# Kernel optimization log

Measured on AMD Instinct MI355X. Metric: run time of the kernel, lower is better.

## Reference

```python
import jax, jax.numpy as jnp
import numpy as np

B = 16; DIM = 256; HEADS = 8; GRID = 64; WS = 8; NQ = 8; POOL = 4
HD = DIM // HEADS
SCALE = HD ** -0.5


def _rel_pos_index(ws):
    coords = np.stack(np.meshgrid(np.arange(ws), np.arange(ws), indexing='ij'))  # (2, ws, ws)
    cf = coords.reshape(2, -1)
    rel = (cf[:, :, None] - cf[:, None, :]).transpose(1, 2, 0).copy()
    rel[:, :, 0] += ws - 1
    rel[:, :, 1] += ws - 1
    rel[:, :, 0] *= 2 * ws - 1
    return rel.sum(-1)  # (ws*ws, ws*ws) int


def layernorm(x, g, b, eps=1e-5):
    m = x.mean(-1, keepdims=True)
    v = ((x - m) ** 2).mean(-1, keepdims=True)
    return (x - m) / jnp.sqrt(v + eps) * g + b


def linear(x, w, b):
    # torch Linear: y = x @ W.T + b, W is (out, in)
    return jnp.einsum('...i,oi->...o', x, w) + b


def setup_inputs() -> dict:
    key = jax.random.key(0)
    ks = iter(jax.random.split(key, 40))
    r = lambda shp, s=0.02: jax.random.normal(next(ks), shp, jnp.float32) * s
    C = DIM
    return {
        'x': jax.random.normal(next(ks), (B, GRID * GRID, C), jnp.float32),
        'query_tokens': r((1, NQ, C)),
        'kproj_w': r((C, C)), 'kproj_b': r((C,)),
        'kbn_g': jnp.ones((C,)), 'kbn_b': jnp.zeros((C,)),
        'kbn_m': jnp.zeros((C,)), 'kbn_v': jnp.ones((C,)),
        'vproj_w': r((C, C)), 'vproj_b': r((C,)),
        'vbn_g': jnp.ones((C,)), 'vbn_b': jnp.zeros((C,)),
        'vbn_m': jnp.zeros((C,)), 'vbn_v': jnp.ones((C,)),
        'ck_w': r((C, C)), 'ck_b': r((C,)),
        'cv_w': r((C, C)), 'cv_b': r((C,)),
        'rpb_table': r(((2 * WS - 1) ** 2, HEADS)),
        'qkv_w': r((3 * C, C)), 'qkv_b': r((3 * C,)),
        'proj_w': r((C, C)), 'proj_b': r((C,)),
        'n1_g': jnp.ones((C,)), 'n1_b': jnp.zeros((C,)),
        'n2_g': jnp.ones((C,)), 'n2_b': jnp.zeros((C,)),
        'fc1_w': r((4 * C, C)), 'fc1_b': r((4 * C,)),
        'fc2_w': r((C, 4 * C)), 'fc2_b': r((C,)),
    }


def reference(x, query_tokens, kproj_w, kproj_b, kbn_g, kbn_b, kbn_m, kbn_v,
              vproj_w, vproj_b, vbn_g, vbn_b, vbn_m, vbn_v,
              ck_w, ck_b, cv_w, cv_b, rpb_table, qkv_w, qkv_b, proj_w, proj_b,
              n1_g, n1_b, n2_g, n2_b, fc1_w, fc1_b, fc2_w, fc2_b):
    Bx, N, C = x.shape
    shortcut = x
    xn = layernorm(x, n1_g, n1_b)

    # ---- global cross-attention pooling path ----
    x2d = xn.reshape(Bx, GRID, GRID, C).transpose(0, 3, 1, 2)  # B,C,H,W
    hp = GRID // POOL
    pooled = x2d.reshape(Bx, C, hp, POOL, hp, POOL).mean((3, 5))  # B,C,hp,hp

    def proj_bn(p, w, b, g, bt, m, v):
        y = jnp.einsum('oc,bchw->bohw', w, p) + b[None, :, None, None]
        y = (y - m[None, :, None, None]) / jnp.sqrt(v + 1e-5)[None, :, None, None]
        y = y * g[None, :, None, None] + bt[None, :, None, None]
        return y.reshape(Bx, C, hp * hp).transpose(0, 2, 1)  # B, hp*hp, C

    k = proj_bn(pooled, kproj_w, kproj_b, kbn_g, kbn_b, kbn_m, kbn_v)
    v = proj_bn(pooled, vproj_w, vproj_b, vbn_g, vbn_b, vbn_m, vbn_v)
    q = jnp.broadcast_to(query_tokens, (Bx, NQ, C))
    qh = q.reshape(Bx, NQ, HEADS, HD).transpose(0, 2, 1, 3)
    kh = k.reshape(Bx, -1, HEADS, HD).transpose(0, 2, 1, 3)
    vh = v.reshape(Bx, -1, HEADS, HD).transpose(0, 2, 1, 3)
    a = jax.nn.softmax(jnp.einsum('bhqd,bhkd->bhqk', qh, kh) * SCALE, axis=-1)
    qout = jnp.einsum('bhqk,bhkd->bhqd', a, vh).transpose(0, 2, 1, 3).reshape(Bx, NQ, C)
    gk = linear(qout + q, ck_w, ck_b)  # B, NQ, C
    gv = linear(qout + q, cv_w, cv_b)

    # ---- window partition ----
    nw = GRID // WS
    xw = xn.reshape(Bx, nw, WS, nw, WS, C).transpose(0, 1, 3, 2, 4, 5).reshape(Bx * nw * nw, WS * WS, C)
    B_, Nw = Bx * nw * nw, WS * WS
    qkv = linear(xw, qkv_w, qkv_b).reshape(B_, Nw, 3, HEADS, HD).transpose(2, 0, 3, 1, 4)
    wq, wk, wv = qkv[0], qkv[1], qkv[2]  # B_, H, Nw, HD

    gkh = jnp.broadcast_to(gk[:, None], (Bx, nw * nw, NQ, C)).reshape(B_, NQ, HEADS, HD).transpose(0, 2, 1, 3)
    gvh = jnp.broadcast_to(gv[:, None], (Bx, nw * nw, NQ, C)).reshape(B_, NQ, HEADS, HD).transpose(0, 2, 1, 3)
    wk = jnp.concatenate([wk, gkh], axis=2)  # kv_len = Nw + NQ
    wv = jnp.concatenate([wv, gvh], axis=2)

    attn = jnp.einsum('bhqd,bhkd->bhqk', wq * SCALE, wk)  # B_, H, Nw, Nw+NQ
    rpi = _rel_pos_index(WS)
    bias = rpb_table[rpi.reshape(-1)].reshape(Nw, Nw, HEADS).transpose(2, 0, 1)  # H, Nw, Nw
    attn = attn.at[:, :, :, :Nw].add(bias[None])
    attn = jax.nn.softmax(attn, axis=-1)
    out = jnp.einsum('bhqk,bhkd->bhqd', attn, wv).transpose(0, 2, 1, 3).reshape(B_, Nw, C)
    out = linear(out, proj_w, proj_b)

    # window reverse
    out = out.reshape(Bx, nw, nw, WS, WS, C).transpose(0, 1, 3, 2, 4, 5).reshape(Bx, N, C)

    x = shortcut + out
    xm = layernorm(x, n2_g, n2_b)
    h = jax.nn.gelu(linear(xm, fc1_w, fc1_b), approximate=False)
    x = x + linear(h, fc2_w, fc2_b)
    return (x, attn)
```

## Files before the change

kernel.cpp:

```cpp
#include <hip/hip_runtime.h>
#include <hip/hip_bf16.h>
#include <math.h>

#define BATCH 16
#define DIM 256
#define HEADS 8
#define HD 32
#define GRID_ 64
#define NTOK 4096
#define WS 8
#define NQ 8
#define POOL 4
#define HP 16
#define NPOOL 256
#define NW 8
#define NWTOK 64
#define KVLEN 72
#define SCALE 0.17677669529663687f

typedef short short8 __attribute__((ext_vector_type(8)));
typedef float f32x4 __attribute__((ext_vector_type(4)));

typedef __hip_bfloat16 bf16;

__device__ inline short f2bf_bits(float f) {
    bf16 h = __float2bfloat16(f);
    return *reinterpret_cast<short*>(&h);
}

__global__ void f2bf_kernel(const float* __restrict__ src, bf16* __restrict__ dst, int n) {
    int i = blockIdx.x * 256 + threadIdx.x;
    if (i < n) dst[i] = __float2bfloat16(src[i]);
}

__device__ inline void store_val(float* p, float v) { *p = v; }
__device__ inline void store_val(bf16* p, float v) { *p = __float2bfloat16(v); }

template <typename OT>
__global__ void ln_kernel(const float* __restrict__ x, const float* __restrict__ g,
                          const float* __restrict__ bb, OT* __restrict__ y) {
    int row = blockIdx.x;
    int t = threadIdx.x;
    float v = x[(size_t)row * 256 + t];
    float s = v, sq = v * v;
    #pragma unroll
    for (int o = 32; o > 0; o >>= 1) {
        s += __shfl_down(s, o);
        sq += __shfl_down(sq, o);
    }
    __shared__ float ls[4], lq[4];
    __shared__ float mean_s, rstd_s;
    int w = t >> 6;
    if ((t & 63) == 0) { ls[w] = s; lq[w] = sq; }
    __syncthreads();
    if (t == 0) {
        float S = ls[0] + ls[1] + ls[2] + ls[3];
        float Q = lq[0] + lq[1] + lq[2] + lq[3];
        float m = S * (1.0f / 256.0f);
        float var = Q * (1.0f / 256.0f) - m * m;
        mean_s = m;
        rstd_s = rsqrtf(var + 1e-5f);
    }
    __syncthreads();
    store_val(&y[(size_t)row * 256 + t], (v - mean_s) * rstd_s * g[t] + bb[t]);
}

__global__ void pool_kernel(const bf16* __restrict__ xn, float* __restrict__ pooled) {
    int bp = blockIdx.x;
    int b = bp >> 8, p = bp & 255;
    int ph = p >> 4, pw = p & 15;
    int c = threadIdx.x;
    float s = 0.f;
    #pragma unroll
    for (int i = 0; i < 4; i++)
        #pragma unroll
        for (int j = 0; j < 4; j++) {
            int n = (ph * 4 + i) * GRID_ + pw * 4 + j;
            s += __bfloat162float(xn[((size_t)b * NTOK + n) * 256 + c]);
        }
    pooled[(size_t)bp * 256 + c] = s * 0.0625f;
}

#define MM_PLAIN 0
#define MM_BN 1
template <int MODE>
__global__ void mm_kernel(const float* __restrict__ A, const float* __restrict__ W,
                          const float* __restrict__ bias, float* __restrict__ out,
                          int K, int N,
                          const float* __restrict__ e0, const float* __restrict__ e1,
                          const float* __restrict__ e2, const float* __restrict__ e3) {
    __shared__ float As[64][17];
    __shared__ float Bs[64][17];
    int t = threadIdx.x;
    int ty = t >> 4, tx = t & 15;
    size_t rowBase = (size_t)blockIdx.y * 64;
    int colBase = blockIdx.x * 64;
    float acc[4][4] = {};
    for (int k0 = 0; k0 < K; k0 += 16) {
        #pragma unroll
        for (int l = 0; l < 4; l++) {
            int e = t + l * 256;
            int r = e >> 4, kk = e & 15;
            As[r][kk] = A[(rowBase + r) * (size_t)K + k0 + kk];
            Bs[r][kk] = W[((size_t)colBase + r) * K + k0 + kk];
        }
        __syncthreads();
        #pragma unroll
        for (int kk = 0; kk < 16; kk++) {
            float a[4], b[4];
            #pragma unroll
            for (int i = 0; i < 4; i++) a[i] = As[ty * 4 + i][kk];
            #pragma unroll
            for (int j = 0; j < 4; j++) b[j] = Bs[tx * 4 + j][kk];
            #pragma unroll
            for (int i = 0; i < 4; i++)
                #pragma unroll
                for (int j = 0; j < 4; j++)
                    acc[i][j] = fmaf(a[i], b[j], acc[i][j]);
        }
        __syncthreads();
    }
    #pragma unroll
    for (int i = 0; i < 4; i++) {
        size_t r = rowBase + ty * 4 + i;
        #pragma unroll
        for (int j = 0; j < 4; j++) {
            int o = colBase + tx * 4 + j;
            float s = acc[i][j] + bias[o];
            if (MODE == MM_BN) {
                s = (s - e0[o]) * rsqrtf(e1[o] + 1e-5f) * e2[o] + e3[o];
            }
            out[r * (size_t)N + o] = s;
        }
    }
}

#define FM_BF16 0
#define FM_GELU 1
#define FM_RES 2
template <int MODE>
__global__ __launch_bounds__(256) void mfma_mm(
    const bf16* __restrict__ A,
    const bf16* __restrict__ W,
    const float* __restrict__ bias,
    void* __restrict__ outv,
    const float* __restrict__ res,
    int K, int N)
{
    __shared__ short Alds[128 * 32];
    __shared__ short Blds[128 * 32];
    int t = threadIdx.x;
    int l = t & 63;
    int w = t >> 6;
    int wm = w >> 1, wn = w & 1;
    size_t rowBase = (size_t)blockIdx.y * 128;
    int colBase = blockIdx.x * 128;
    const short* Ag = (const short*)A;
    const short* Wg = (const short*)W;

    f32x4 acc[4][4];
    #pragma unroll
    for (int i = 0; i < 4; i++)
        #pragma unroll
        for (int j = 0; j < 4; j++)
            acc[i][j] = (f32x4){0.f, 0.f, 0.f, 0.f};

    int quad = l >> 4, lm = l & 15;

    for (int k0 = 0; k0 < K; k0 += 32) {
        __syncthreads();
        #pragma unroll
        for (int it = 0; it < 2; it++) {
            int u = it * 256 + t;
            int r = u & 127, q = u >> 7;
            __builtin_amdgcn_global_load_lds(
                (const __attribute__((address_space(1))) void*)(Ag + (rowBase + r) * (size_t)K + k0 + q * 8),
                (__attribute__((address_space(3))) void*)(&Alds[u * 8]), 16, 0, 0);
            __builtin_amdgcn_global_load_lds(
                (const __attribute__((address_space(1))) void*)(Wg + ((size_t)colBase + r) * K + k0 + q * 8),
                (__attribute__((address_space(3))) void*)(&Blds[u * 8]), 16, 0, 0);
        }
        __syncthreads();

        short8 afrag[4], bfrag[4];
        #pragma unroll
        for (int mt = 0; mt < 4; mt++) {
            int row = wm * 64 + mt * 16 + lm;
            afrag[mt] = *(const short8*)&Alds[(quad * 128 + row) * 8];
        }
        #pragma unroll
        for (int nt = 0; nt < 4; nt++) {
            int col = wn * 64 + nt * 16 + lm;
            bfrag[nt] = *(const short8*)&Blds[(quad * 128 + col) * 8];
        }
        #pragma unroll
        for (int mt = 0; mt < 4; mt++)
            #pragma unroll
            for (int nt = 0; nt < 4; nt++)
                acc[mt][nt] = __builtin_amdgcn_mfma_f32_16x16x32_bf16(
                    afrag[mt], bfrag[nt], acc[mt][nt], 0, 0, 0);
    }

    #pragma unroll
    for (int mt = 0; mt < 4; mt++) {
        #pragma unroll
        for (int nt = 0; nt < 4; nt++) {
            int col = colBase + wn * 64 + nt * 16 + lm;
            float bcol = bias[col];
            f32x4 a = acc[mt][nt];
            #pragma unroll
            for (int r = 0; r < 4; r++) {
                size_t row = rowBase + wm * 64 + mt * 16 + quad * 4 + r;
                float s = a[r] + bcol;
                if (MODE == FM_GELU) {
                    s = 0.5f * s * (1.0f + erff(s * 0.70710678118654752f));
                }
                if (MODE == FM_RES) {
                    s += res[row * (size_t)N + col];
                    ((float*)outv)[row * (size_t)N + col] = s;
                } else {
                    ((bf16*)outv)[row * (size_t)N + col] = __float2bfloat16(s);
                }
            }
        }
    }
}

__global__ void cross_attn_kernel(const float* __restrict__ qtok,
                                  const float* __restrict__ k,
                                  const float* __restrict__ v,
                                  float* __restrict__ qoutq) {
    int b = blockIdx.x >> 3, h = blockIdx.x & 7;
    int t = threadIdx.x;
    __shared__ float qs[8][32];
    __shared__ float sc[8][257];
    {
        int i = t >> 5, d = t & 31;
        qs[i][d] = qtok[i * 256 + h * 32 + d];
    }
    __syncthreads();
    {
        const float* kp = k + ((size_t)b * NPOOL + t) * 256 + h * 32;
        float kd[32];
        #pragma unroll
        for (int d = 0; d < 32; d++) kd[d] = kp[d];
        #pragma unroll
        for (int i = 0; i < 8; i++) {
            float s = 0.f;
            #pragma unroll
            for (int d = 0; d < 32; d++) s += qs[i][d] * kd[d];
            sc[i][t] = s * SCALE;
        }
    }
    __syncthreads();
    {
        int r = t >> 5, ln = t & 31;
        float mx = -1e30f;
        for (int j = ln; j < 256; j += 32) mx = fmaxf(mx, sc[r][j]);
        #pragma unroll
        for (int o = 16; o > 0; o >>= 1) mx = fmaxf(mx, __shfl_xor(mx, o));
        float sum = 0.f;
        for (int j = ln; j < 256; j += 32) {
            float e = __expf(sc[r][j] - mx);
            sc[r][j] = e;
            sum += e;
        }
        #pragma unroll
        for (int o = 16; o > 0; o >>= 1) sum += __shfl_xor(sum, o);
        float inv = 1.f / sum;
        for (int j = ln; j < 256; j += 32) sc[r][j] *= inv;
    }
    __syncthreads();
    {
        int i = t >> 5, d = t & 31;
        float acc = 0.f;
        for (int j = 0; j < 256; j++)
            acc += sc[i][j] * v[((size_t)b * NPOOL + j) * 256 + h * 32 + d];
        qoutq[((size_t)b * NQ + i) * 256 + h * 32 + d] = acc + qs[i][d];
    }
}

#define QS_S 72
#define KS_S 72
#define VS_S 80
#define PS_S 104
__global__ __launch_bounds__(256) void win_attn_mfma(
    const bf16* __restrict__ qkv,
    const float* __restrict__ gk,
    const float* __restrict__ gv,
    const float* __restrict__ rpb,
    float* __restrict__ attn_out,
    bf16* __restrict__ attno)
{
    int blk = blockIdx.x;
    int w = blk >> 2, hp = blk & 3;
    int b = w >> 6, wi = w & 63;
    int wy = wi >> 3, wx = wi & 7;
    int t = threadIdx.x;
    int lane = t & 63, wv = t >> 6;
    int hl = wv >> 1;
    int h = hp * 2 + hl;
    int msel = wv & 1;
    int lm = lane & 15, q4 = lane >> 4;

    __shared__ __attribute__((aligned(16))) short smem[2 * 64 * PS_S + KVLEN * VS_S];
    short* ps = smem;
    short* qs = smem;
    short* ks = smem + 64 * QS_S;
    short* vs = smem + 2 * 64 * PS_S;

    const short* qkvp = (const short*)qkv;
    for (int u = t; u < 1536; u += 256) {
        int seg = u >> 9;
        int r = (u >> 3) & 63;
        int c = u & 7;
        int n = (wy * 8 + (r >> 3)) * GRID_ + wx * 8 + (r & 7);
        short8 val = *(const short8*)(qkvp + ((size_t)(b * NTOK + n)) * 768 + seg * 256 + hp * 64 + c * 8);
        short* dst = (seg == 0) ? &qs[r * QS_S + c * 8]
                   : (seg == 1) ? &ks[r * KS_S + c * 8]
                                : &vs[r * VS_S + c * 8];
        *(short8*)dst = val;
    }
    for (int idx = t; idx < 512; idx += 256) {
        int i = idx >> 6, d = idx & 63;
        float gkv = gk[((size_t)b * NQ + i) * 256 + hp * 64 + d];
        float gvv = gv[((size_t)b * NQ + i) * 256 + hp * 64 + d];
        ks[(64 + i) * KS_S + d] = f2bf_bits(gkv);
        vs[(64 + i) * VS_S + d] = f2bf_bits(gvv);
    }
    __syncthreads();

    f32x4 acc[2][5];
    #pragma unroll
    for (int mt = 0; mt < 2; mt++)
        #pragma unroll
        for (int nt = 0; nt < 5; nt++)
            acc[mt][nt] = (f32x4){0.f, 0.f, 0.f, 0.f};

    short8 afrag[2], bfrag[5];
    #pragma unroll
    for (int mt = 0; mt < 2; mt++) {
        int row = msel * 32 + mt * 16 + lm;
        afrag[mt] = *(const short8*)&qs[row * QS_S + hl * 32 + q4 * 8];
    }
    #pragma unroll
    for (int nt = 0; nt < 5; nt++) {
        int col = nt * 16 + lm;
        int jc = (col < KVLEN) ? col : 0;
        bfrag[nt] = *(const short8*)&ks[jc * KS_S + hl * 32 + q4 * 8];
    }
    #pragma unroll
    for (int mt = 0; mt < 2; mt++)
        #pragma unroll
        for (int nt = 0; nt < 5; nt++)
            acc[mt][nt] = __builtin_amdgcn_mfma_f32_16x16x32_bf16(
                afrag[mt], bfrag[nt], acc[mt][nt], 0, 0, 0);

    #pragma unroll
    for (int mt = 0; mt < 2; mt++) {
        #pragma unroll
        for (int r = 0; r < 4; r++) {
            int rowl = msel * 32 + mt * 16 + q4 * 4 + r;
            int yi = rowl >> 3, xi = rowl & 7;
            float sv[5];
            float mx = -1e30f;
            #pragma unroll
            for (int nt = 0; nt < 5; nt++) {
                float s = acc[mt][nt][r] * SCALE;
                int j = nt * 16 + lm;
                if (j < 64) {
                    int rpi = (yi - (j >> 3) + 7) * 15 + (xi - (j & 7) + 7);
                    s += rpb[rpi * 8 + h];
                } else if (j >= KVLEN) {
                    s = -1e30f;
                }
                sv[nt] = s;
                mx = fmaxf(mx, s);
            }
            #pragma unroll
            for (int o = 1; o < 16; o <<= 1) mx = fmaxf(mx, __shfl_xor(mx, o));
            float sum = 0.f;
            #pragma unroll
            for (int nt = 0; nt < 5; nt++) {
                float e = __expf(sv[nt] - mx);
                sv[nt] = e;
                sum += e;
            }
            #pragma unroll
            for (int o = 1; o < 16; o <<= 1) sum += __shfl_xor(sum, o);
            float inv = 1.f / sum;
            #pragma unroll
            for (int nt = 0; nt < 5; nt++) acc[mt][nt][r] = sv[nt] * inv;
        }
    }

    __syncthreads();

    size_t abase = ((size_t)(w * 8 + h)) * (64 * KVLEN);
    #pragma unroll
    for (int mt = 0; mt < 2; mt++) {
        #pragma unroll
        for (int r = 0; r < 4; r++) {
            int rowl = msel * 32 + mt * 16 + q4 * 4 + r;
            #pragma unroll
            for (int nt = 0; nt < 5; nt++) {
                int j = nt * 16 + lm;
                float p = acc[mt][nt][r];
                if (j < KVLEN) attn_out[abase + rowl * KVLEN + j] = p;
                ps[(hl * 64 + rowl) * PS_S + j] = f2bf_bits(p);
            }
        }
    }
    if (t < 128) {
        int hh = t >> 6, rr = t & 63;
        short8 z = {};
        *(short8*)&ps[(hh * 64 + rr) * PS_S + 80] = z;
        *(short8*)&ps[(hh * 64 + rr) * PS_S + 88] = z;
    }
    __syncthreads();

    f32x4 oacc[2][2];
    #pragma unroll
    for (int mt = 0; mt < 2; mt++)
        #pragma unroll
        for (int nt = 0; nt < 2; nt++)
            oacc[mt][nt] = (f32x4){0.f, 0.f, 0.f, 0.f};

    #pragma unroll
    for (int kc = 0; kc < 3; kc++) {
        short8 pa[2];
        #pragma unroll
        for (int mt = 0; mt < 2; mt++) {
            int row = msel * 32 + mt * 16 + lm;
            pa[mt] = *(const short8*)&ps[(hl * 64 + row) * PS_S + kc * 32 + q4 * 8];
        }
        #pragma unroll
        for (int nt = 0; nt < 2; nt++) {
            int d = hl * 32 + nt * 16 + lm;
            short8 bv;
            #pragma unroll
            for (int e = 0; e < 8; e++) {
                int k = kc * 32 + q4 * 8 + e;
                int kk = (k < KVLEN) ? k : 0;
                bv[e] = vs[kk * VS_S + d];
            }
            #pragma unroll
            for (int mt = 0; mt < 2; mt++)
                oacc[mt][nt] = __builtin_amdgcn_mfma_f32_16x16x32_bf16(
                    pa[mt], bv, oacc[mt][nt], 0, 0, 0);
        }
    }

    #pragma unroll
    for (int mt = 0; mt < 2; mt++) {
        #pragma unroll
        for (int nt = 0; nt < 2; nt++) {
            #pragma unroll
            for (int r = 0; r < 4; r++) {
                int rowl = msel * 32 + mt * 16 + q4 * 4 + r;
                int n = (wy * 8 + (rowl >> 3)) * GRID_ + wx * 8 + (rowl & 7);
                attno[((size_t)(b * NTOK + n)) * 256 + h * 32 + nt * 16 + lm] =
                    __float2bfloat16(oacc[mt][nt][r]);
            }
        }
    }
}

extern "C" void kernel_launch(void* const* d_in, const int* in_sizes, int n_in,
                              void* d_out, int out_size, void* d_ws, size_t ws_size,
                              hipStream_t stream) {
    const float* x       = (const float*)d_in[0];
    const float* qtok    = (const float*)d_in[1];
    const float* kproj_w = (const float*)d_in[2];
    const float* kproj_b = (const float*)d_in[3];
    const float* kbn_g   = (const float*)d_in[4];
    const float* kbn_b   = (const float*)d_in[5];
    const float* kbn_m   = (const float*)d_in[6];
    const float* kbn_v   = (const float*)d_in[7];
    const float* vproj_w = (const float*)d_in[8];
    const float* vproj_b = (const float*)d_in[9];
    const float* vbn_g   = (const float*)d_in[10];
    const float* vbn_b   = (const float*)d_in[11];
    const float* vbn_m   = (const float*)d_in[12];
    const float* vbn_v   = (const float*)d_in[13];
    const float* ck_w    = (const float*)d_in[14];
    const float* ck_b    = (const float*)d_in[15];
    const float* cv_w    = (const float*)d_in[16];
    const float* cv_b    = (const float*)d_in[17];
    const float* rpb     = (const float*)d_in[18];
    const float* qkv_w   = (const float*)d_in[19];
    const float* qkv_b   = (const float*)d_in[20];
    const float* proj_w  = (const float*)d_in[21];
    const float* proj_b  = (const float*)d_in[22];
    const float* n1_g    = (const float*)d_in[23];
    const float* n1_b    = (const float*)d_in[24];
    const float* n2_g    = (const float*)d_in[25];
    const float* n2_b    = (const float*)d_in[26];
    const float* fc1_w   = (const float*)d_in[27];
    const float* fc1_b   = (const float*)d_in[28];
    const float* fc2_w   = (const float*)d_in[29];
    const float* fc2_b   = (const float*)d_in[30];

    float* out_x    = (float*)d_out;
    float* out_attn = (float*)d_out + (size_t)BATCH * NTOK * DIM;

    const size_t ROWS = (size_t)BATCH * NTOK;

    bf16* xn    = (bf16*)d_ws;
    bf16* qkvb  = xn + ROWS * 256;
    bf16* attno = qkvb + ROWS * 768;
    bf16* hbuf  = qkvb;
    bf16* wqkv  = attno + ROWS * 256;
    bf16* wproj = wqkv + 196608;
    bf16* wfc1  = wproj + 65536;
    bf16* wfc2  = wfc1 + 262144;
    float* pooled = (float*)(wfc2 + 262144);
    float* kbuf   = pooled + 1048576;
    float* vbuf   = kbuf + 1048576;
    float* qoutq  = vbuf + 1048576;
    float* gkbuf  = qoutq + 32768;
    float* gvbuf  = gkbuf + 32768;
    bf16* xm = xn;

    f2bf_kernel<<<dim3(768), dim3(256), 0, stream>>>(qkv_w, wqkv, 196608);
    f2bf_kernel<<<dim3(256), dim3(256), 0, stream>>>(proj_w, wproj, 65536);
    f2bf_kernel<<<dim3(1024), dim3(256), 0, stream>>>(fc1_w, wfc1, 262144);
    f2bf_kernel<<<dim3(1024), dim3(256), 0, stream>>>(fc2_w, wfc2, 262144);
    ln_kernel<bf16><<<dim3(ROWS), dim3(256), 0, stream>>>(x, n1_g, n1_b, xn);
    pool_kernel<<<dim3(BATCH * NPOOL), dim3(256), 0, stream>>>(xn, pooled);
    mm_kernel<MM_BN><<<dim3(4, 64), dim3(256), 0, stream>>>(
        pooled, kproj_w, kproj_b, kbuf, 256, 256, kbn_m, kbn_v, kbn_g, kbn_b);
    mm_kernel<MM_BN><<<dim3(4, 64), dim3(256), 0, stream>>>(
        pooled, vproj_w, vproj_b, vbuf, 256, 256, vbn_m, vbn_v, vbn_g, vbn_b);
    cross_attn_kernel<<<dim3(BATCH * HEADS), dim3(256), 0, stream>>>(qtok, kbuf, vbuf, qoutq);
    mm_kernel<MM_PLAIN><<<dim3(4, 2), dim3(256), 0, stream>>>(
        qoutq, ck_w, ck_b, gkbuf, 256, 256, nullptr, nullptr, nullptr, nullptr);
    mm_kernel<MM_PLAIN><<<dim3(4, 2), dim3(256), 0, stream>>>(
        qoutq, cv_w, cv_b, gvbuf, 256, 256, nullptr, nullptr, nullptr, nullptr);
    mfma_mm<FM_BF16><<<dim3(6, 512), dim3(256), 0, stream>>>(
        xn, wqkv, qkv_b, qkvb, nullptr, 256, 768);
    win_attn_mfma<<<dim3(1024 * 4), dim3(256), 0, stream>>>(
        qkvb, gkbuf, gvbuf, rpb, out_attn, attno);
    mfma_mm<FM_RES><<<dim3(2, 512), dim3(256), 0, stream>>>(
        attno, wproj, proj_b, out_x, x, 256, 256);
    ln_kernel<bf16><<<dim3(ROWS), dim3(256), 0, stream>>>(out_x, n2_g, n2_b, xm);
    mfma_mm<FM_GELU><<<dim3(8, 512), dim3(256), 0, stream>>>(
        xm, wfc1, fc1_b, hbuf, nullptr, 256, 1024);
    mfma_mm<FM_RES><<<dim3(2, 512), dim3(256), 0, stream>>>(
        hbuf, wfc2, fc2_b, out_x, out_x, 1024, 256);
}
```

Baseline: 885.3 us.

## Fuse proj+residual+LayerNorm, double-buffer GEMM LDS, merge weight casts, cache RPB in LDS

Fuses the output projection, residual add and second LayerNorm into one full-row (256-column) MFMA kernel, which removes one full pass over out_x. Double-buffers the LDS tiles in the generic MFMA GEMM so the next K slice loads while the current one computes, at the cost of twice the shared memory. Merges the four weight-cast launches into one kernel and unrolls the cross-attention PV loop. Stages the relative-position bias table as bf16 in window-attention shared memory, which slightly lowers bias precision and reuses part of the smem region.

```diff
diff --git a/kernel.cpp b/kernel.cpp
--- a/kernel.cpp
+++ b/kernel.cpp
@@ -27,10 +27,24 @@
     bf16 h = __float2bfloat16(f);
     return *reinterpret_cast<short*>(&h);
 }
-
-__global__ void f2bf_kernel(const float* __restrict__ src, bf16* __restrict__ dst, int n) {
+__device__ inline float bfbits2f(short s) {
+    return __bfloat162float(*reinterpret_cast<bf16*>(&s));
+}
+
+__global__ void f2bf4_kernel(const float* __restrict__ s0, bf16* __restrict__ d0,
+                             const float* __restrict__ s1, bf16* __restrict__ d1,
+                             const float* __restrict__ s2, bf16* __restrict__ d2,
+                             const float* __restrict__ s3, bf16* __restrict__ d3) {
     int i = blockIdx.x * 256 + threadIdx.x;
-    if (i < n) dst[i] = __float2bfloat16(src[i]);
+    if (i < 196608) {
+        d0[i] = __float2bfloat16(s0[i]);
+    } else if (i < 262144) {
+        int j = i - 196608; d1[j] = __float2bfloat16(s1[j]);
+    } else if (i < 524288) {
+        int j = i - 262144; d2[j] = __float2bfloat16(s2[j]);
+    } else {
+        int j = i - 524288; d3[j] = __float2bfloat16(s3[j]);
+    }
 }
 
 __device__ inline void store_val(float* p, float v) { *p = v; }
@@ -147,8 +161,8 @@
     const float* __restrict__ res,
     int K, int N)
 {
-    __shared__ short Alds[128 * 32];
-    __shared__ short Blds[128 * 32];
+    __shared__ short Alds[2][128 * 32];
+    __shared__ short Blds[2][128 * 32];
     int t = threadIdx.x;
     int l = t & 63;
     int w = t >> 6;
@@ -167,31 +181,37 @@
 
     int quad = l >> 4, lm = l & 15;
 
-    for (int k0 = 0; k0 < K; k0 += 32) {
-        __syncthreads();
+    auto stage = [&](int buf, int k0) {
         #pragma unroll
         for (int it = 0; it < 2; it++) {
             int u = it * 256 + t;
             int r = u & 127, q = u >> 7;
             __builtin_amdgcn_global_load_lds(
                 (const __attribute__((address_space(1))) void*)(Ag + (rowBase + r) * (size_t)K + k0 + q * 8),
-                (__attribute__((address_space(3))) void*)(&Alds[u * 8]), 16, 0, 0);
+                (__attribute__((address_space(3))) void*)(&Alds[buf][u * 8]), 16, 0, 0);
             __builtin_amdgcn_global_load_lds(
                 (const __attribute__((address_space(1))) void*)(Wg + ((size_t)colBase + r) * K + k0 + q * 8),
-                (__attribute__((address_space(3))) void*)(&Blds[u * 8]), 16, 0, 0);
-        }
-        __syncthreads();
+                (__attribute__((address_space(3))) void*)(&Blds[buf][u * 8]), 16, 0, 0);
+        }
+    };
+
+    stage(0, 0);
+    __syncthreads();
+    int nk = K >> 5;
+    for (int kt = 0; kt < nk; kt++) {
+        int buf = kt & 1;
+        if (kt + 1 < nk) stage(buf ^ 1, (kt + 1) << 5);
 
         short8 afrag[4], bfrag[4];
         #pragma unroll
         for (int mt = 0; mt < 4; mt++) {
             int row = wm * 64 + mt * 16 + lm;
-            afrag[mt] = *(const short8*)&Alds[(quad * 128 + row) * 8];
+            afrag[mt] = *(const short8*)&Alds[buf][(quad * 128 + row) * 8];
         }
         #pragma unroll
         for (int nt = 0; nt < 4; nt++) {
             int col = wn * 64 + nt * 16 + lm;
-            bfrag[nt] = *(const short8*)&Blds[(quad * 128 + col) * 8];
+            bfrag[nt] = *(const short8*)&Blds[buf][(quad * 128 + col) * 8];
         }
         #pragma unroll
         for (int mt = 0; mt < 4; mt++)
@@ -199,6 +219,7 @@
             for (int nt = 0; nt < 4; nt++)
                 acc[mt][nt] = __builtin_amdgcn_mfma_f32_16x16x32_bf16(
                     afrag[mt], bfrag[nt], acc[mt][nt], 0, 0, 0);
+        __syncthreads();
     }
 
     #pragma unroll
@@ -226,6 +247,116 @@
     }
 }
 
+__global__ __launch_bounds__(256) void proj_res_ln(
+    const bf16* __restrict__ A,
+    const bf16* __restrict__ W,
+    const float* __restrict__ bias,
+    const float* __restrict__ res,
+    const float* __restrict__ g,
+    const float* __restrict__ bb,
+    float* __restrict__ outx,
+    bf16* __restrict__ xm)
+{
+    __shared__ short Alds[2][128 * 32];
+    __shared__ short Blds[2][256 * 32];
+    int t = threadIdx.x;
+    int lane = t & 63, w = t >> 6;
+    int quad = lane >> 4, lm = lane & 15;
+    size_t rowBase = (size_t)blockIdx.x * 128;
+    const short* Ag = (const short*)A;
+    const short* Wg = (const short*)W;
+
+    f32x4 acc[2][16];
+    #pragma unroll
+    for (int mt = 0; mt < 2; mt++)
+        #pragma unroll
+        for (int nt = 0; nt < 16; nt++)
+            acc[mt][nt] = (f32x4){0.f, 0.f, 0.f, 0.f};
+
+    auto stage = [&](int buf, int k0) {
+        #pragma unroll
+        for (int it = 0; it < 2; it++) {
+            int u = it * 256 + t;
+            int r = u & 127, q = u >> 7;
+            __builtin_amdgcn_global_load_lds(
+                (const __attribute__((address_space(1))) void*)(Ag + (rowBase + r) * 256 + k0 + q * 8),
+                (__attribute__((address_space(3))) void*)(&Alds[buf][u * 8]), 16, 0, 0);
+        }
+        #pragma unroll
+        for (int it = 0; it < 4; it++) {
+            int u = it * 256 + t;
+            int r = u & 255, q = u >> 8;
+            __builtin_amdgcn_global_load_lds(
+                (const __attribute__((address_space(1))) void*)(Wg + (size_t)r * 256 + k0 + q * 8),
+                (__attribute__((address_space(3))) void*)(&Blds[buf][u * 8]), 16, 0, 0);
+        }
+    };
+
+    stage(0, 0);
+    __syncthreads();
+    #pragma unroll 1
+    for (int kt = 0; kt < 8; kt++) {
+        int buf = kt & 1;
+        if (kt < 7) stage(buf ^ 1, (kt + 1) * 32);
+        short8 af[2];
+        #pragma unroll
+        for (int mt = 0; mt < 2; mt++) {
+            int row = w * 32 + mt * 16 + lm;
+            af[mt] = *(const short8*)&Alds[buf][(quad * 128 + row) * 8];
+        }
+        #pragma unroll
+        for (int nt = 0; nt < 16; nt++) {
+            int col = nt * 16 + lm;
+            short8 bfv = *(const short8*)&Blds[buf][(quad * 256 + col) * 8];
+            #pragma unroll
+            for (int mt = 0; mt < 2; mt++)
+                acc[mt][nt] = __builtin_amdgcn_mfma_f32_16x16x32_bf16(
+                    af[mt], bfv, acc[mt][nt], 0, 0, 0);
+        }
+        __syncthreads();
+    }
+
+    float biasr[16], gr[16], br2[16];
+    #pragma unroll
+    for (int nt = 0; nt < 16; nt++) {
+        int col = nt * 16 + lm;
+        biasr[nt] = bias[col];
+        gr[nt] = g[col];
+        br2[nt] = bb[col];
+    }
+    #pragma unroll
+    for (int mt = 0; mt < 2; mt++) {
+        #pragma unroll
+        for (int r = 0; r < 4; r++) {
+            size_t row = rowBase + w * 32 + mt * 16 + quad * 4 + r;
+            float sum = 0.f, sq = 0.f;
+            #pragma unroll
+            for (int nt = 0; nt < 16; nt++) {
+                int col = nt * 16 + lm;
+                float s = acc[mt][nt][r] + biasr[nt] + res[row * 256 + col];
+                acc[mt][nt][r] = s;
+                sum += s;
+                sq += s * s;
+            }
+            #pragma unroll
+            for (int o = 1; o < 16; o <<= 1) {
+                sum += __shfl_xor(sum, o);
+                sq += __shfl_xor(sq, o);
+            }
+            float m = sum * (1.0f / 256.0f);
+            float var = sq * (1.0f / 256.0f) - m * m;
+            float rstd = rsqrtf(var + 1e-5f);
+            #pragma unroll
+            for (int nt = 0; nt < 16; nt++) {
+                int col = nt * 16 + lm;
+                float s = acc[mt][nt][r];
+                outx[row * 256 + col] = s;
+                xm[row * 256 + col] = __float2bfloat16((s - m) * rstd * gr[nt] + br2[nt]);
+            }
+        }
+    }
+}
+
 __global__ void cross_attn_kernel(const float* __restrict__ qtok,
                                   const float* __restrict__ k,
                                   const float* __restrict__ v,
@@ -274,6 +405,7 @@
     {
         int i = t >> 5, d = t & 31;
         float acc = 0.f;
+        #pragma unroll 4
         for (int j = 0; j < 256; j++)
             acc += sc[i][j] * v[((size_t)b * NPOOL + j) * 256 + h * 32 + d];
         qoutq[((size_t)b * NQ + i) * 256 + h * 32 + d] = acc + qs[i][d];
@@ -307,6 +439,7 @@
     short* ps = smem;
     short* qs = smem;
     short* ks = smem + 64 * QS_S;
+    short* rpbs = smem + 9792;
     short* vs = smem + 2 * 64 * PS_S;
 
     const short* qkvp = (const short*)qkv;
@@ -321,6 +454,7 @@
                                 : &vs[r * VS_S + c * 8];
         *(short8*)dst = val;
     }
+    for (int i = t; i < 1800; i += 256) rpbs[i] = f2bf_bits(rpb[i]);
     for (int idx = t; idx < 512; idx += 256) {
         int i = idx >> 6, d = idx & 63;
         float gkv = gk[((size_t)b * NQ + i) * 256 + hp * 64 + d];
@@ -370,7 +504,7 @@
                 int j = nt * 16 + lm;
                 if (j < 64) {
                     int rpi = (yi - (j >> 3) + 7) * 15 + (xi - (j & 7) + 7);
-                    s += rpb[rpi * 8 + h];
+                    s += bfbits2f(rpbs[rpi * 8 + h]);
                 } else if (j >= KVLEN) {
                     s = -1e30f;
                 }
@@ -522,10 +656,8 @@
     float* gvbuf  = gkbuf + 32768;
     bf16* xm = xn;
 
-    f2bf_kernel<<<dim3(768), dim3(256), 0, stream>>>(qkv_w, wqkv, 196608);
-    f2bf_kernel<<<dim3(256), dim3(256), 0, stream>>>(proj_w, wproj, 65536);
-    f2bf_kernel<<<dim3(1024), dim3(256), 0, stream>>>(fc1_w, wfc1, 262144);
-    f2bf_kernel<<<dim3(1024), dim3(256), 0, stream>>>(fc2_w, wfc2, 262144);
+    f2bf4_kernel<<<dim3(3072), dim3(256), 0, stream>>>(
+        qkv_w, wqkv, proj_w, wproj, fc1_w, wfc1, fc2_w, wfc2);
     ln_kernel<bf16><<<dim3(ROWS), dim3(256), 0, stream>>>(x, n1_g, n1_b, xn);
     pool_kernel<<<dim3(BATCH * NPOOL), dim3(256), 0, stream>>>(xn, pooled);
     mm_kernel<MM_BN><<<dim3(4, 64), dim3(256), 0, stream>>>(
@@ -541,9 +673,8 @@
         xn, wqkv, qkv_b, qkvb, nullptr, 256, 768);
     win_attn_mfma<<<dim3(1024 * 4), dim3(256), 0, stream>>>(
         qkvb, gkbuf, gvbuf, rpb, out_attn, attno);
-    mfma_mm<FM_RES><<<dim3(2, 512), dim3(256), 0, stream>>>(
-        attno, wproj, proj_b, out_x, x, 256, 256);
-    ln_kernel<bf16><<<dim3(ROWS), dim3(256), 0, stream>>>(out_x, n2_g, n2_b, xm);
+    proj_res_ln<<<dim3(512), dim3(256), 0, stream>>>(
+        attno, wproj, proj_b, x, n2_g, n2_b, out_x, xm);
     mfma_mm<FM_GELU><<<dim3(8, 512), dim3(256), 0, stream>>>(
         xm, wfc1, fc1_b, hbuf, nullptr, 256, 1024);
     mfma_mm<FM_RES><<<dim3(2, 512), dim3(256), 0, stream>>>(
```

Result: faster. 865.7 us (-2.2%).
